# Optimization experiments

Measured on AMD Instinct MI355X. Metric: run time of the kernel, lower is better.

Reference implementation:

```python
import jax, jax.numpy as jnp
import numpy as np

N = 100000   # number of vertices
E = 20000    # number of hyperedges
NNZ = 1000000  # incidence entries
D = 64
ALPHA = 0.5
BETA = 0.5


def setup_inputs() -> dict:
    key = jax.random.key(0)
    ks = jax.random.split(key, 8)
    s = 1.0 / np.sqrt(D)
    return {
        "X": jax.random.normal(ks[0], (N, D), dtype=jnp.float32),
        "X0": jax.random.normal(ks[1], (N, D), dtype=jnp.float32),
        "W1": jax.random.normal(ks[2], (D, D), dtype=jnp.float32) * s,
        "b1": jnp.zeros((D,), dtype=jnp.float32),
        "W2": jax.random.normal(ks[3], (D, D), dtype=jnp.float32) * s,
        "b2": jnp.zeros((D,), dtype=jnp.float32),
        "vertex": jax.random.randint(ks[4], (NNZ,), 0, N),
        "edges": jax.random.randint(ks[5], (NNZ,), 0, E),
    }


def reference(X, X0, W1, b1, W2, b2, vertex, edges):
    # vertex -> edge aggregation (scatter-add)
    Xve = X[vertex]                                    # [nnz, D]
    Xe = jax.ops.segment_sum(Xve, edges, num_segments=E)   # [E, D]
    # edge -> vertex aggregation
    Xev = Xe[edges]                                    # [nnz, D]
    Xv = jax.ops.segment_sum(Xev, vertex, num_segments=N)  # [N, D]
    # jump link residual + MLP
    Xi = (1.0 - ALPHA) * Xv + ALPHA * X0
    h = jax.nn.relu(Xi @ W1 + b1)
    mlp = h @ W2 + b2
    return (1.0 - BETA) * Xi + BETA * mlp
```

## Files before the change

### kernel.cpp

```cpp
#include <hip/hip_runtime.h>

#define NV    100000
#define NE    20000
#define NNZT  1000000
#define DIM   64

#define EBITS 4
#define ELOC  16
#define EBK   (NE / ELOC)
#define CAP_E 1024
#define ESH   17
#define EMASK 0x1FFFF

#define VBITS 6
#define VLOC  64
#define VBK   ((NV + VLOC - 1) / VLOC)
#define CAP_V 896
#define VSH   15
#define VMASK 0x7FFF

#define CHUNK 4096
#define NBIN  ((NNZT + CHUNK - 1) / CHUNK)

typedef __attribute__((ext_vector_type(8))) short bf16x8;
typedef __attribute__((ext_vector_type(4))) float f32x4;

__device__ __forceinline__ float bf2f(unsigned short u) {
    return __uint_as_float(((unsigned)u) << 16);
}
__device__ __forceinline__ unsigned short f2bf(float f) {
    unsigned u = __float_as_uint(f);
    u += 0x7FFF + ((u >> 16) & 1);
    return (unsigned short)(u >> 16);
}

__global__ __launch_bounds__(256) void bin_kernel(
    const int* __restrict__ vertex, const int* __restrict__ edges,
    int* __restrict__ ecur, int* __restrict__ vcur,
    unsigned int* __restrict__ erecs, unsigned int* __restrict__ vrecs) {
    __shared__ int hE[EBK], hV[VBK];
    __shared__ int cE[EBK], cV[VBK];
    int tid = threadIdx.x;
    for (int t = tid; t < EBK; t += 256) hE[t] = 0;
    for (int t = tid; t < VBK; t += 256) hV[t] = 0;
    __syncthreads();
    int base4 = blockIdx.x * (CHUNK / 4);
    #pragma unroll
    for (int k = 0; k < CHUNK / 4 / 256; k++) {
        int i = base4 + k * 256 + tid;
        if (i < NNZT / 4) {
            int4 e = ((const int4*)edges)[i];
            int4 v = ((const int4*)vertex)[i];
            atomicAdd(&hE[e.x >> EBITS], 1); atomicAdd(&hE[e.y >> EBITS], 1);
            atomicAdd(&hE[e.z >> EBITS], 1); atomicAdd(&hE[e.w >> EBITS], 1);
            atomicAdd(&hV[v.x >> VBITS], 1); atomicAdd(&hV[v.y >> VBITS], 1);
            atomicAdd(&hV[v.z >> VBITS], 1); atomicAdd(&hV[v.w >> VBITS], 1);
        }
    }
    __syncthreads();
    for (int t = tid; t < EBK; t += 256) { int h = hE[t]; cE[t] = h ? atomicAdd(&ecur[t], h) : 0; }
    for (int t = tid; t < VBK; t += 256) { int h = hV[t]; cV[t] = h ? atomicAdd(&vcur[t], h) : 0; }
    __syncthreads();
    #pragma unroll
    for (int k = 0; k < CHUNK / 4 / 256; k++) {
        int i = base4 + k * 256 + tid;
        if (i < NNZT / 4) {
            int4 e = ((const int4*)edges)[i];
            int4 v = ((const int4*)vertex)[i];
            int be, bv, p;
            be = e.x >> EBITS; p = atomicAdd(&cE[be], 1); if (p < CAP_E) erecs[be * CAP_E + p] = ((unsigned)(e.x & 15) << ESH) | (unsigned)v.x;
            be = e.y >> EBITS; p = atomicAdd(&cE[be], 1); if (p < CAP_E) erecs[be * CAP_E + p] = ((unsigned)(e.y & 15) << ESH) | (unsigned)v.y;
            be = e.z >> EBITS; p = atomicAdd(&cE[be], 1); if (p < CAP_E) erecs[be * CAP_E + p] = ((unsigned)(e.z & 15) << ESH) | (unsigned)v.z;
            be = e.w >> EBITS; p = atomicAdd(&cE[be], 1); if (p < CAP_E) erecs[be * CAP_E + p] = ((unsigned)(e.w & 15) << ESH) | (unsigned)v.w;
            bv = v.x >> VBITS; p = atomicAdd(&cV[bv], 1); if (p < CAP_V) vrecs[bv * CAP_V + p] = ((unsigned)(v.x & 63) << VSH) | (unsigned)e.x;
            bv = v.y >> VBITS; p = atomicAdd(&cV[bv], 1); if (p < CAP_V) vrecs[bv * CAP_V + p] = ((unsigned)(v.y & 63) << VSH) | (unsigned)e.y;
            bv = v.z >> VBITS; p = atomicAdd(&cV[bv], 1); if (p < CAP_V) vrecs[bv * CAP_V + p] = ((unsigned)(v.z & 63) << VSH) | (unsigned)e.z;
            bv = v.w >> VBITS; p = atomicAdd(&cV[bv], 1); if (p < CAP_V) vrecs[bv * CAP_V + p] = ((unsigned)(v.w & 63) << VSH) | (unsigned)e.w;
        }
    }
}

__global__ __launch_bounds__(256) void conv_w(
    const float* __restrict__ W1, const float* __restrict__ W2,
    unsigned short* __restrict__ W1T, unsigned short* __restrict__ W2T) {
    int tid = threadIdx.x;
    for (int t = tid; t < DIM * DIM; t += 256) {
        int k = t >> 6, n = t & 63;
        W1T[n * DIM + k] = f2bf(W1[k * DIM + n]);
        W2T[n * DIM + k] = f2bf(W2[k * DIM + n]);
    }
}

__global__ __launch_bounds__(256, 4) void agg_edges_srt(
    const float* __restrict__ X,
    const int* __restrict__ ebc, const unsigned int* __restrict__ erecs,
    unsigned short* __restrict__ Xeb) {
    __shared__ int rbuf[CAP_E];
    __shared__ int sbuf[CAP_E];
    __shared__ int boff[ELOC + 1];
    __shared__ int bcur[ELOC];
    int tid = threadIdx.x;
    int b = blockIdx.x;
    int cnt = ebc[b]; if (cnt > CAP_E) cnt = CAP_E;
    const unsigned int* src = erecs + (size_t)b * CAP_E;
    for (int t = tid; t < cnt; t += 256) rbuf[t] = (int)src[t];
    if (tid < ELOC) bcur[tid] = 0;
    __syncthreads();
    for (int t = tid; t < cnt; t += 256) atomicAdd(&bcur[((unsigned)rbuf[t]) >> ESH], 1);
    __syncthreads();
    if (tid == 0) {
        int run = 0;
        for (int i = 0; i < ELOC; i++) { int c = bcur[i]; boff[i] = run; bcur[i] = run; run += c; }
        boff[ELOC] = run;
    }
    __syncthreads();
    for (int t = tid; t < cnt; t += 256) {
        unsigned r = (unsigned)rbuf[t];
        int p = atomicAdd(&bcur[r >> ESH], 1);
        sbuf[p] = (int)(r & EMASK);
    }
    __syncthreads();

    int wave = tid >> 6, lane = tid & 63;
    #pragma unroll
    for (int q = 0; q < 4; q++) {
        int le = wave * 4 + q;
        int beg = boff[le], end = boff[le + 1];
        float acc = 0.f;
        int j = beg;
        for (; j + 8 <= end; j += 8) {
            int v0 = sbuf[j],     v1 = sbuf[j + 1], v2 = sbuf[j + 2], v3 = sbuf[j + 3];
            int v4 = sbuf[j + 4], v5 = sbuf[j + 5], v6 = sbuf[j + 6], v7 = sbuf[j + 7];
            float a0 = X[v0 * DIM + lane], a1 = X[v1 * DIM + lane];
            float a2 = X[v2 * DIM + lane], a3 = X[v3 * DIM + lane];
            float a4 = X[v4 * DIM + lane], a5 = X[v5 * DIM + lane];
            float a6 = X[v6 * DIM + lane], a7 = X[v7 * DIM + lane];
            acc += ((a0 + a1) + (a2 + a3)) + ((a4 + a5) + (a6 + a7));
        }
        for (; j + 4 <= end; j += 4) {
            int v0 = sbuf[j], v1 = sbuf[j + 1], v2 = sbuf[j + 2], v3 = sbuf[j + 3];
            float a0 = X[v0 * DIM + lane], a1 = X[v1 * DIM + lane];
            float a2 = X[v2 * DIM + lane], a3 = X[v3 * DIM + lane];
            acc += (a0 + a1) + (a2 + a3);
        }
        for (; j < end; j++) acc += X[sbuf[j] * DIM + lane];
        Xeb[(size_t)(b * ELOC + le) * DIM + lane] = f2bf(acc);
    }
}

__global__ __launch_bounds__(256) void agg_verts_srt(
    const unsigned short* __restrict__ Xeb, const float* __restrict__ X0,
    const int* __restrict__ vbc, const unsigned int* __restrict__ vrecs,
    float* __restrict__ xi_out) {
    __shared__ int rbuf[CAP_V];
    __shared__ int sbuf[CAP_V];
    __shared__ int boff[VLOC + 1];
    __shared__ int bcur[VLOC];
    int tid = threadIdx.x;
    int b = blockIdx.x;
    int cnt = vbc[b]; if (cnt > CAP_V) cnt = CAP_V;
    const unsigned int* src = vrecs + (size_t)b * CAP_V;
    for (int t = tid; t < cnt; t += 256) rbuf[t] = (int)src[t];
    if (tid < VLOC) bcur[tid] = 0;
    __syncthreads();
    for (int t = tid; t < cnt; t += 256) atomicAdd(&bcur[((unsigned)rbuf[t]) >> VSH], 1);
    __syncthreads();
    if (tid == 0) {
        int run = 0;
        for (int i = 0; i < VLOC; i++) { int c = bcur[i]; boff[i] = run; bcur[i] = run; run += c; }
        boff[VLOC] = run;
    }
    __syncthreads();
    for (int t = tid; t < cnt; t += 256) {
        unsigned r = (unsigned)rbuf[t];
        int p = atomicAdd(&bcur[r >> VSH], 1);
        sbuf[p] = (int)(r & VMASK);
    }
    __syncthreads();

    int wave = tid >> 6, lane = tid & 63;
    int row0 = b << VBITS;
    for (int q = 0; q < 16; q++) {
        int lv = wave * 16 + q;
        int row = row0 + lv;
        if (row >= NV) break;
        int beg = boff[lv], end = boff[lv + 1];
        float acc = 0.f;
        int j = beg;
        for (; j + 8 <= end; j += 8) {
            int e0 = sbuf[j],     e1 = sbuf[j + 1], e2 = sbuf[j + 2], e3 = sbuf[j + 3];
            int e4 = sbuf[j + 4], e5 = sbuf[j + 5], e6 = sbuf[j + 6], e7 = sbuf[j + 7];
            float a0 = bf2f(Xeb[e0 * DIM + lane]), a1 = bf2f(Xeb[e1 * DIM + lane]);
            float a2 = bf2f(Xeb[e2 * DIM + lane]), a3 = bf2f(Xeb[e3 * DIM + lane]);
            float a4 = bf2f(Xeb[e4 * DIM + lane]), a5 = bf2f(Xeb[e5 * DIM + lane]);
            float a6 = bf2f(Xeb[e6 * DIM + lane]), a7 = bf2f(Xeb[e7 * DIM + lane]);
            acc += ((a0 + a1) + (a2 + a3)) + ((a4 + a5) + (a6 + a7));
        }
        for (; j + 4 <= end; j += 4) {
            int e0 = sbuf[j], e1 = sbuf[j + 1], e2 = sbuf[j + 2], e3 = sbuf[j + 3];
            float a0 = bf2f(Xeb[e0 * DIM + lane]), a1 = bf2f(Xeb[e1 * DIM + lane]);
            float a2 = bf2f(Xeb[e2 * DIM + lane]), a3 = bf2f(Xeb[e3 * DIM + lane]);
            acc += (a0 + a1) + (a2 + a3);
        }
        for (; j < end; j++) acc += bf2f(Xeb[sbuf[j] * DIM + lane]);
        float xi = 0.5f * acc + 0.5f * X0[(size_t)row * DIM + lane];
        xi_out[(size_t)row * DIM + lane] = xi;
    }
}

__global__ __launch_bounds__(256) void mlp_mfma(
    const unsigned short* __restrict__ W1T, const unsigned short* __restrict__ W2T,
    const float* __restrict__ b1, const float* __restrict__ b2,
    float* __restrict__ io) {
    __shared__ __align__(16) unsigned short sW1[DIM * DIM];
    __shared__ __align__(16) unsigned short sW2[DIM * DIM];
    __shared__ __align__(16) unsigned short ht[4][16 * 72];
    int tid = threadIdx.x;
    for (int t = tid; t < DIM * DIM / 8; t += 256) {
        ((bf16x8*)sW1)[t] = ((const bf16x8*)W1T)[t];
        ((bf16x8*)sW2)[t] = ((const bf16x8*)W2T)[t];
    }
    __syncthreads();

    int wave = tid >> 6, lane = tid & 63;
    int m = lane & 15, quad = lane >> 4;
    int row0 = blockIdx.x * 64 + wave * 16;

    int arow = row0 + m;
    bool avalid = (arow < NV);
    const float* xrow = io + (size_t)(avalid ? arow : 0) * DIM;
    bf16x8 a0, a1;
    #pragma unroll
    for (int j = 0; j < 8; j++) {
        float x0 = avalid ? xrow[quad * 8 + j] : 0.f;
        float x1 = avalid ? xrow[32 + quad * 8 + j] : 0.f;
        a0[j] = (short)f2bf(x0);
        a1[j] = (short)f2bf(x1);
    }

    f32x4 h[4];
    #pragma unroll
    for (int nt = 0; nt < 4; nt++) {
        float bias = b1[nt * 16 + m];
        f32x4 c = {bias, bias, bias, bias};
        const bf16x8* wb = (const bf16x8*)(sW1 + (nt * 16 + m) * DIM);
        c = __builtin_amdgcn_mfma_f32_16x16x32_bf16(a0, wb[quad], c, 0, 0, 0);
        c = __builtin_amdgcn_mfma_f32_16x16x32_bf16(a1, wb[4 + quad], c, 0, 0, 0);
        h[nt] = c;
    }

    unsigned short* hw = ht[wave];
    #pragma unroll
    for (int nt = 0; nt < 4; nt++) {
        #pragma unroll
        for (int r = 0; r < 4; r++) {
            float v = fmaxf(h[nt][r], 0.f);
            hw[(quad * 4 + r) * 72 + nt * 16 + m] = f2bf(v);
        }
    }
    __syncthreads();

    bf16x8 g0 = *(const bf16x8*)(hw + m * 72 + quad * 8);
    bf16x8 g1 = *(const bf16x8*)(hw + m * 72 + 32 + quad * 8);

    f32x4 o[4];
    #pragma unroll
    for (int nt = 0; nt < 4; nt++) {
        float bias = b2[nt * 16 + m];
        f32x4 c = {bias, bias, bias, bias};
        const bf16x8* wb = (const bf16x8*)(sW2 + (nt * 16 + m) * DIM);
        c = __builtin_amdgcn_mfma_f32_16x16x32_bf16(g0, wb[quad], c, 0, 0, 0);
        c = __builtin_amdgcn_mfma_f32_16x16x32_bf16(g1, wb[4 + quad], c, 0, 0, 0);
        o[nt] = c;
    }

    #pragma unroll
    for (int nt = 0; nt < 4; nt++) {
        #pragma unroll
        for (int r = 0; r < 4; r++) {
            int row = row0 + quad * 4 + r;
            if (row < NV) {
                size_t idx = (size_t)row * DIM + nt * 16 + m;
                float xi = io[idx];
                io[idx] = 0.5f * xi + 0.5f * o[nt][r];
            }
        }
    }
}

extern "C" void kernel_launch(void* const* d_in, const int* in_sizes, int n_in,
                              void* d_out, int out_size, void* d_ws, size_t ws_size,
                              hipStream_t stream) {
    const float* X  = (const float*)d_in[0];
    const float* X0 = (const float*)d_in[1];
    const float* W1 = (const float*)d_in[2];
    const float* b1 = (const float*)d_in[3];
    const float* W2 = (const float*)d_in[4];
    const float* b2 = (const float*)d_in[5];
    const int* vertex = (const int*)d_in[6];
    const int* edges  = (const int*)d_in[7];
    float* out = (float*)d_out;

    char* p = (char*)d_ws;
    int* ecur = (int*)p;                          p += (size_t)EBK * 4;
    int* vcur = (int*)p;                          p += (size_t)VBK * 4;
    p = (char*)(((uintptr_t)p + 15) & ~(uintptr_t)15);
    unsigned int* erecs = (unsigned int*)p;       p += (size_t)EBK * CAP_E * 4;
    unsigned int* vrecs = (unsigned int*)p;       p += (size_t)VBK * CAP_V * 4;
    unsigned short* Xeb = (unsigned short*)p;     p += (size_t)NE * DIM * 2;
    unsigned short* W1T = (unsigned short*)p;     p += (size_t)DIM * DIM * 2;
    unsigned short* W2T = (unsigned short*)p;     p += (size_t)DIM * DIM * 2;

    hipMemsetAsync(d_ws, 0, (size_t)(EBK + VBK) * sizeof(int), stream);

    dim3 blk(256);
    bin_kernel<<<NBIN, blk, 0, stream>>>(vertex, edges, ecur, vcur, erecs, vrecs);
    conv_w<<<1, blk, 0, stream>>>(W1, W2, W1T, W2T);
    agg_edges_srt<<<EBK, blk, 0, stream>>>(X, ecur, erecs, Xeb);
    agg_verts_srt<<<VBK, blk, 0, stream>>>(Xeb, X0, vcur, vrecs, out);
    mlp_mfma<<<(NV + 63) / 64, blk, 0, stream>>>(W1T, W2T, b1, b2, out);
}
```

Baseline: 233.8 us.

## Fuse vertex aggregation with MLP and parallelize bucket prefix scan

Merges the edge-to-vertex aggregation kernel with the MFMA MLP kernel, so the jump-link result Xi stays in shared memory instead of being written to global memory and read back. This removes one launch and a full N×D fp32 round trip. Each block now also loads both weight matrices into shared memory and holds a 64x68 fp32 Xi tile, which raises LDS use per block and may lower occupancy. The serial single-thread prefix sum over buckets is replaced with a wave shuffle scan in both aggregation kernels.

```diff
diff --git a/kernel.cpp b/kernel.cpp
--- a/kernel.cpp
+++ b/kernel.cpp
@@ -21,6 +21,8 @@
 
 #define CHUNK 4096
 #define NBIN  ((NNZT + CHUNK - 1) / CHUNK)
+
+#define XSTR  68
 
 typedef __attribute__((ext_vector_type(8))) short bf16x8;
 typedef __attribute__((ext_vector_type(4))) float f32x4;
@@ -108,10 +110,17 @@
     __syncthreads();
     for (int t = tid; t < cnt; t += 256) atomicAdd(&bcur[((unsigned)rbuf[t]) >> ESH], 1);
     __syncthreads();
-    if (tid == 0) {
-        int run = 0;
-        for (int i = 0; i < ELOC; i++) { int c = bcur[i]; boff[i] = run; bcur[i] = run; run += c; }
-        boff[ELOC] = run;
+    if (tid < ELOC) {
+        int c = bcur[tid];
+        int x = c;
+        #pragma unroll
+        for (int ofs = 1; ofs < ELOC; ofs <<= 1) {
+            int y = __shfl_up(x, ofs, 64);
+            if (tid >= ofs) x += y;
+        }
+        boff[tid + 1] = x;
+        if (tid == 0) boff[0] = 0;
+        bcur[tid] = x - c;
     }
     __syncthreads();
     for (int t = tid; t < cnt; t += 256) {
@@ -148,27 +157,44 @@
     }
 }
 
-__global__ __launch_bounds__(256) void agg_verts_srt(
+__global__ __launch_bounds__(256) void agg_verts_mlp_mfma(
     const unsigned short* __restrict__ Xeb, const float* __restrict__ X0,
+    const unsigned short* __restrict__ W1T, const unsigned short* __restrict__ W2T,
+    const float* __restrict__ b1, const float* __restrict__ b2,
     const int* __restrict__ vbc, const unsigned int* __restrict__ vrecs,
-    float* __restrict__ xi_out) {
+    float* __restrict__ out) {
     __shared__ int rbuf[CAP_V];
     __shared__ int sbuf[CAP_V];
     __shared__ int boff[VLOC + 1];
     __shared__ int bcur[VLOC];
+    __shared__ __align__(16) unsigned short sW1[DIM * DIM];
+    __shared__ __align__(16) unsigned short sW2[DIM * DIM];
+    __shared__ __align__(16) float xif[VLOC * XSTR];
+    __shared__ __align__(16) unsigned short ht[4][16 * 72];
     int tid = threadIdx.x;
     int b = blockIdx.x;
     int cnt = vbc[b]; if (cnt > CAP_V) cnt = CAP_V;
     const unsigned int* src = vrecs + (size_t)b * CAP_V;
     for (int t = tid; t < cnt; t += 256) rbuf[t] = (int)src[t];
+    for (int t = tid; t < DIM * DIM / 8; t += 256) {
+        ((bf16x8*)sW1)[t] = ((const bf16x8*)W1T)[t];
+        ((bf16x8*)sW2)[t] = ((const bf16x8*)W2T)[t];
+    }
     if (tid < VLOC) bcur[tid] = 0;
     __syncthreads();
     for (int t = tid; t < cnt; t += 256) atomicAdd(&bcur[((unsigned)rbuf[t]) >> VSH], 1);
     __syncthreads();
-    if (tid == 0) {
-        int run = 0;
-        for (int i = 0; i < VLOC; i++) { int c = bcur[i]; boff[i] = run; bcur[i] = run; run += c; }
-        boff[VLOC] = run;
+    if (tid < VLOC) {
+        int c = bcur[tid];
+        int x = c;
+        #pragma unroll
+        for (int ofs = 1; ofs < VLOC; ofs <<= 1) {
+            int y = __shfl_up(x, ofs, 64);
+            if (tid >= ofs) x += y;
+        }
+        boff[tid + 1] = x;
+        if (tid == 0) boff[0] = 0;
+        bcur[tid] = x - c;
     }
     __syncthreads();
     for (int t = tid; t < cnt; t += 256) {
@@ -183,60 +209,48 @@
     for (int q = 0; q < 16; q++) {
         int lv = wave * 16 + q;
         int row = row0 + lv;
-        if (row >= NV) break;
-        int beg = boff[lv], end = boff[lv + 1];
-        float acc = 0.f;
-        int j = beg;
-        for (; j + 8 <= end; j += 8) {
-            int e0 = sbuf[j],     e1 = sbuf[j + 1], e2 = sbuf[j + 2], e3 = sbuf[j + 3];
-            int e4 = sbuf[j + 4], e5 = sbuf[j + 5], e6 = sbuf[j + 6], e7 = sbuf[j + 7];
-            float a0 = bf2f(Xeb[e0 * DIM + lane]), a1 = bf2f(Xeb[e1 * DIM + lane]);
-            float a2 = bf2f(Xeb[e2 * DIM + lane]), a3 = bf2f(Xeb[e3 * DIM + lane]);
-            float a4 = bf2f(Xeb[e4 * DIM + lane]), a5 = bf2f(Xeb[e5 * DIM + lane]);
-            float a6 = bf2f(Xeb[e6 * DIM + lane]), a7 = bf2f(Xeb[e7 * DIM + lane]);
-            acc += ((a0 + a1) + (a2 + a3)) + ((a4 + a5) + (a6 + a7));
-        }
-        for (; j + 4 <= end; j += 4) {
-            int e0 = sbuf[j], e1 = sbuf[j + 1], e2 = sbuf[j + 2], e3 = sbuf[j + 3];
-            float a0 = bf2f(Xeb[e0 * DIM + lane]), a1 = bf2f(Xeb[e1 * DIM + lane]);
-            float a2 = bf2f(Xeb[e2 * DIM + lane]), a3 = bf2f(Xeb[e3 * DIM + lane]);
-            acc += (a0 + a1) + (a2 + a3);
-        }
-        for (; j < end; j++) acc += bf2f(Xeb[sbuf[j] * DIM + lane]);
-        float xi = 0.5f * acc + 0.5f * X0[(size_t)row * DIM + lane];
-        xi_out[(size_t)row * DIM + lane] = xi;
-    }
-}
-
-__global__ __launch_bounds__(256) void mlp_mfma(
-    const unsigned short* __restrict__ W1T, const unsigned short* __restrict__ W2T,
-    const float* __restrict__ b1, const float* __restrict__ b2,
-    float* __restrict__ io) {
-    __shared__ __align__(16) unsigned short sW1[DIM * DIM];
-    __shared__ __align__(16) unsigned short sW2[DIM * DIM];
-    __shared__ __align__(16) unsigned short ht[4][16 * 72];
-    int tid = threadIdx.x;
-    for (int t = tid; t < DIM * DIM / 8; t += 256) {
-        ((bf16x8*)sW1)[t] = ((const bf16x8*)W1T)[t];
-        ((bf16x8*)sW2)[t] = ((const bf16x8*)W2T)[t];
-    }
-    __syncthreads();
-
-    int wave = tid >> 6, lane = tid & 63;
+        float xi = 0.f;
+        if (row < NV) {
+            int beg = boff[lv], end = boff[lv + 1];
+            float acc = 0.f;
+            int j = beg;
+            for (; j + 8 <= end; j += 8) {
+                int e0 = sbuf[j],     e1 = sbuf[j + 1], e2 = sbuf[j + 2], e3 = sbuf[j + 3];
+                int e4 = sbuf[j + 4], e5 = sbuf[j + 5], e6 = sbuf[j + 6], e7 = sbuf[j + 7];
+                float a0 = bf2f(Xeb[e0 * DIM + lane]), a1 = bf2f(Xeb[e1 * DIM + lane]);
+                float a2 = bf2f(Xeb[e2 * DIM + lane]), a3 = bf2f(Xeb[e3 * DIM + lane]);
+                float a4 = bf2f(Xeb[e4 * DIM + lane]), a5 = bf2f(Xeb[e5 * DIM + lane]);
+                float a6 = bf2f(Xeb[e6 * DIM + lane]), a7 = bf2f(Xeb[e7 * DIM + lane]);
+                acc += ((a0 + a1) + (a2 + a3)) + ((a4 + a5) + (a6 + a7));
+            }
+            for (; j + 4 <= end; j += 4) {
+                int e0 = sbuf[j], e1 = sbuf[j + 1], e2 = sbuf[j + 2], e3 = sbuf[j + 3];
+                float a0 = bf2f(Xeb[e0 * DIM + lane]), a1 = bf2f(Xeb[e1 * DIM + lane]);
+                float a2 = bf2f(Xeb[e2 * DIM + lane]), a3 = bf2f(Xeb[e3 * DIM + lane]);
+                acc += (a0 + a1) + (a2 + a3);
+            }
+            for (; j < end; j++) acc += bf2f(Xeb[sbuf[j] * DIM + lane]);
+            xi = 0.5f * acc + 0.5f * X0[(size_t)row * DIM + lane];
+        }
+        xif[lv * XSTR + lane] = xi;
+    }
+    __builtin_amdgcn_wave_barrier();
+
     int m = lane & 15, quad = lane >> 4;
-    int row0 = blockIdx.x * 64 + wave * 16;
-
-    int arow = row0 + m;
-    bool avalid = (arow < NV);
-    const float* xrow = io + (size_t)(avalid ? arow : 0) * DIM;
+    const float* xrow = xif + (wave * 16 + m) * XSTR;
+    float4 xa0 = *(const float4*)(xrow + quad * 8);
+    float4 xa1 = *(const float4*)(xrow + quad * 8 + 4);
+    float4 xa2 = *(const float4*)(xrow + 32 + quad * 8);
+    float4 xa3 = *(const float4*)(xrow + 32 + quad * 8 + 4);
     bf16x8 a0, a1;
-    #pragma unroll
-    for (int j = 0; j < 8; j++) {
-        float x0 = avalid ? xrow[quad * 8 + j] : 0.f;
-        float x1 = avalid ? xrow[32 + quad * 8 + j] : 0.f;
-        a0[j] = (short)f2bf(x0);
-        a1[j] = (short)f2bf(x1);
-    }
+    a0[0] = (short)f2bf(xa0.x); a0[1] = (short)f2bf(xa0.y);
+    a0[2] = (short)f2bf(xa0.z); a0[3] = (short)f2bf(xa0.w);
+    a0[4] = (short)f2bf(xa1.x); a0[5] = (short)f2bf(xa1.y);
+    a0[6] = (short)f2bf(xa1.z); a0[7] = (short)f2bf(xa1.w);
+    a1[0] = (short)f2bf(xa2.x); a1[1] = (short)f2bf(xa2.y);
+    a1[2] = (short)f2bf(xa2.z); a1[3] = (short)f2bf(xa2.w);
+    a1[4] = (short)f2bf(xa3.x); a1[5] = (short)f2bf(xa3.y);
+    a1[6] = (short)f2bf(xa3.z); a1[7] = (short)f2bf(xa3.w);
 
     f32x4 h[4];
     #pragma unroll
@@ -258,8 +272,7 @@
             hw[(quad * 4 + r) * 72 + nt * 16 + m] = f2bf(v);
         }
     }
-    __syncthreads();
-
+    __builtin_amdgcn_wave_barrier();
     bf16x8 g0 = *(const bf16x8*)(hw + m * 72 + quad * 8);
     bf16x8 g1 = *(const bf16x8*)(hw + m * 72 + 32 + quad * 8);
 
@@ -278,11 +291,11 @@
     for (int nt = 0; nt < 4; nt++) {
         #pragma unroll
         for (int r = 0; r < 4; r++) {
-            int row = row0 + quad * 4 + r;
+            int lrow = wave * 16 + quad * 4 + r;
+            int row = row0 + lrow;
             if (row < NV) {
-                size_t idx = (size_t)row * DIM + nt * 16 + m;
-                float xi = io[idx];
-                io[idx] = 0.5f * xi + 0.5f * o[nt][r];
+                float xi = xif[lrow * XSTR + nt * 16 + m];
+                out[(size_t)row * DIM + nt * 16 + m] = 0.5f * xi + 0.5f * o[nt][r];
             }
         }
     }
@@ -317,6 +330,6 @@
     bin_kernel<<<NBIN, blk, 0, stream>>>(vertex, edges, ecur, vcur, erecs, vrecs);
     conv_w<<<1, blk, 0, stream>>>(W1, W2, W1T, W2T);
     agg_edges_srt<<<EBK, blk, 0, stream>>>(X, ecur, erecs, Xeb);
-    agg_verts_srt<<<VBK, blk, 0, stream>>>(Xeb, X0, vcur, vrecs, out);
-    mlp_mfma<<<(NV + 63) / 64, blk, 0, stream>>>(W1T, W2T, b1, b2, out);
-}
+    agg_verts_mlp_mfma<<<VBK, blk, 0, stream>>>(Xeb, X0, W1T, W2T, b1, b2,
+                                                vcur, vrecs, out);
+}
```

Result: slower. 252.0 us (+7.8%).
